# Optimization experiments

Hardware: AMD Instinct MI355X
Metric: run time of the kernel (lower is better)

The kernel has to match this reference:

```python
import jax, jax.numpy as jnp
import numpy as np

N_NODES = 50000
N_EDGES = 800000
IN_CH = 64
HID = 64
N_LAYERS = 4


def setup_inputs() -> dict:
    key = jax.random.key(0)
    ks = jax.random.split(key, 10)
    x = jax.random.normal(ks[0], (N_NODES, IN_CH), dtype=jnp.float32)
    edge_index = jax.random.randint(ks[1], (2, N_EDGES), 0, N_NODES, dtype=jnp.int32)
    # SAGEConv params per layer: lin_l (applied to aggregated neighbors, with bias)
    # and lin_r (applied to root node). All layers are 64->64 so stack to [L, in, out].
    s = 1.0 / np.sqrt(IN_CH)
    Wl = jax.random.uniform(ks[2], (N_LAYERS, IN_CH, HID), jnp.float32, -s, s)
    Wr = jax.random.uniform(ks[3], (N_LAYERS, IN_CH, HID), jnp.float32, -s, s)
    b = jax.random.uniform(ks[4], (N_LAYERS, HID), jnp.float32, -s, s)
    alpha = jnp.full((N_LAYERS, HID), 0.25, dtype=jnp.float32)  # PReLU init
    return {"x": x, "edge_index": edge_index, "Wl": Wl, "Wr": Wr, "b": b, "alpha": alpha}


def _sage_layer(x, src, dst, deg_inv, Wl, Wr, b):
    # mean aggregation of source-node features at destination nodes
    agg = jax.ops.segment_sum(x[src], dst, num_segments=N_NODES)  # [N, d]
    agg = agg * deg_inv[:, None]
    return agg @ Wl + x @ Wr + b


def _prelu(x, a):
    return jnp.where(x >= 0, x, a * x)


def reference(x, edge_index, Wl, Wr, b, alpha):
    src, dst = edge_index[0], edge_index[1]
    deg = jax.ops.segment_sum(jnp.ones((N_EDGES,), jnp.float32), dst, num_segments=N_NODES)
    deg_inv = 1.0 / jnp.maximum(deg, 1.0)
    for i in range(N_LAYERS):
        x = _sage_layer(x, src, dst, deg_inv, Wl[i], Wr[i], b[i])
        x = _prelu(x, alpha[i])
    return x
```

## Files before the change

### kernel.cpp

```cpp
#include <hip/hip_runtime.h>

#define NN 50000
#define NE 800000
#define C 64
#define NL 4
#define SCAN_NB 196
#define NBK 196
#define HBLK 782

typedef __attribute__((ext_vector_type(8))) short bf16x8;
typedef __attribute__((ext_vector_type(4))) float f32x4;

__device__ __forceinline__ unsigned short f2bf(float f) {
    unsigned u = __float_as_uint(f);
    u += 0x7fffu + ((u >> 16) & 1u);
    return (unsigned short)(u >> 16);
}
__device__ __forceinline__ float4 bf4_to_f4(uint2 p) {
    float4 r;
    r.x = __uint_as_float(p.x << 16);
    r.y = __uint_as_float(p.x & 0xffff0000u);
    r.z = __uint_as_float(p.y << 16);
    r.w = __uint_as_float(p.y & 0xffff0000u);
    return r;
}

__global__ __launch_bounds__(1024) void bucket_hist_kernel(const int* __restrict__ dst,
                                                           int* __restrict__ blk_cnt,
                                                           int* __restrict__ lrank) {
    __shared__ int cnt[NBK];
    int tid = threadIdx.x;
    int blk = blockIdx.x;
    if (tid < NBK) cnt[tid] = 0;
    __syncthreads();
    int e = blk * 1024 + tid;
    if (e < NE) lrank[e] = atomicAdd(&cnt[dst[e] >> 8], 1);
    __syncthreads();
    if (tid < NBK) blk_cnt[tid * HBLK + blk] = cnt[tid];
}

__global__ __launch_bounds__(1024) void scanblk_kernel(int* __restrict__ blk_cnt,
                                                       int* __restrict__ bucket_tot) {
    __shared__ int sdata[1024];
    int b = blockIdx.x;
    int tid = threadIdx.x;
    int v = (tid < HBLK) ? blk_cnt[b * HBLK + tid] : 0;
    sdata[tid] = v;
    __syncthreads();
    for (int off = 1; off < 1024; off <<= 1) {
        int t = (tid >= off) ? sdata[tid - off] : 0;
        __syncthreads();
        sdata[tid] += t;
        __syncthreads();
    }
    if (tid < HBLK) blk_cnt[b * HBLK + tid] = sdata[tid] - v;
    if (tid == HBLK - 1) bucket_tot[b] = sdata[tid];
}

__global__ __launch_bounds__(256) void scanbucket_kernel(const int* __restrict__ bucket_tot,
                                                         int* __restrict__ bucket_start) {
    __shared__ int sdata[256];
    int tid = threadIdx.x;
    int v = (tid < NBK) ? bucket_tot[tid] : 0;
    sdata[tid] = v;
    __syncthreads();
    for (int off = 1; off < 256; off <<= 1) {
        int t = (tid >= off) ? sdata[tid - off] : 0;
        __syncthreads();
        sdata[tid] += t;
        __syncthreads();
    }
    if (tid < NBK) bucket_start[tid] = sdata[tid] - v;
    if (tid == NBK - 1) bucket_start[NBK] = sdata[tid];
}

__global__ __launch_bounds__(1024) void bucket_scatter_kernel(
    const int* __restrict__ src, const int* __restrict__ dst,
    const int* __restrict__ lrank, const int* __restrict__ base2,
    const int* __restrict__ bucket_start, int2* __restrict__ sorted) {
    int blk = blockIdx.x;
    int e = blk * 1024 + threadIdx.x;
    if (e < NE) {
        int d = dst[e];
        int b = d >> 8;
        int pos = bucket_start[b] + base2[b * HBLK + blk] + lrank[e];
        sorted[pos] = make_int2(src[e], d);
    }
}

__global__ __launch_bounds__(512) void bucket_deg_kernel(const int2* __restrict__ sorted,
                                                         const int* __restrict__ bucket_start,
                                                         int* __restrict__ deg) {
    __shared__ int ldeg[256];
    int b = blockIdx.x;
    int tid = threadIdx.x;
    if (tid < 256) ldeg[tid] = 0;
    __syncthreads();
    int lo = bucket_start[b], hi = bucket_start[b + 1];
    for (int i = lo + tid; i < hi; i += 512)
        atomicAdd(&ldeg[sorted[i].y & 255], 1);
    __syncthreads();
    if (tid < 256) deg[b * 256 + tid] = ldeg[tid];
}

__global__ __launch_bounds__(256) void scan1_kernel(const int* __restrict__ deg,
                                                    int* __restrict__ row_start,
                                                    int* __restrict__ bsums) {
    __shared__ int sdata[256];
    int tid = threadIdx.x;
    int i = blockIdx.x * 256 + tid;
    int v = (i < NN) ? deg[i] : 0;
    sdata[tid] = v;
    __syncthreads();
    for (int off = 1; off < 256; off <<= 1) {
        int t = (tid >= off) ? sdata[tid - off] : 0;
        __syncthreads();
        sdata[tid] += t;
        __syncthreads();
    }
    int incl = sdata[tid];
    if (i < NN) row_start[i] = incl - v;
    if (tid == 255) bsums[blockIdx.x] = incl;
}

__global__ __launch_bounds__(256) void scan23_kernel(int* __restrict__ row_start,
                                                     const int* __restrict__ bsums,
                                                     const int* __restrict__ deg,
                                                     float* __restrict__ deg_inv) {
    __shared__ int sdata[256];
    int tid = threadIdx.x;
    int v = (tid < SCAN_NB) ? bsums[tid] : 0;
    sdata[tid] = v;
    __syncthreads();
    for (int off = 1; off < 256; off <<= 1) {
        int t = (tid >= off) ? sdata[tid - off] : 0;
        __syncthreads();
        sdata[tid] += t;
        __syncthreads();
    }
    int b = blockIdx.x;
    int offset = (b == 0) ? 0 : sdata[b - 1];
    int i = b * 256 + tid;
    if (i < NN) {
        row_start[i] += offset;
        deg_inv[i] = 1.0f / fmaxf((float)deg[i], 1.0f);
    }
}

__global__ __launch_bounds__(512) void bucket_fill_kernel(const int2* __restrict__ sorted,
                                                          const int* __restrict__ bucket_start,
                                                          const int* __restrict__ row_start,
                                                          int* __restrict__ csr_src) {
    __shared__ int rs[256];
    __shared__ int lcnt[256];
    int b = blockIdx.x;
    int tid = threadIdx.x;
    if (tid < 256) {
        int n = b * 256 + tid;
        rs[tid] = (n < NN) ? row_start[n] : 0;
        lcnt[tid] = 0;
    }
    __syncthreads();
    int lo = bucket_start[b], hi = bucket_start[b + 1];
    for (int i = lo + tid; i < hi; i += 512) {
        int2 p = sorted[i];
        int r = atomicAdd(&lcnt[p.y & 255], 1);
        csr_src[rs[p.y & 255] + r] = p.x;
    }
}

__global__ __launch_bounds__(512) void transform_mfma_kernel(
    const float* __restrict__ xin,
    const float* __restrict__ Wl, const float* __restrict__ Wr,
    const float* __restrict__ bias,
    unsigned short* __restrict__ y, float* __restrict__ z)
{
    __shared__ unsigned short xs[64][72];
    __shared__ unsigned short wlT[64][72];
    __shared__ unsigned short wrT[64][72];
    __shared__ unsigned short ys[64][64];
    __shared__ float zs[64][64];
    __shared__ float bs[C];

    int tid = threadIdx.x;
    int node0 = blockIdx.x * 64;

    for (int i = tid; i < C * C; i += 512) {
        int k = i >> 6, c = i & 63;
        wlT[c][k] = f2bf(Wl[i]);
        wrT[c][k] = f2bf(Wr[i]);
    }
    if (tid < C) bs[tid] = bias[tid];
    for (int i = tid; i < 64 * 16; i += 512) {
        int nl = i >> 4, c4 = i & 15;
        int n = node0 + nl;
        int nc = n < NN ? n : NN - 1;
        float4 v = ((const float4*)xin)[(size_t)nc * 16 + c4];
        xs[nl][c4 * 4 + 0] = f2bf(v.x);
        xs[nl][c4 * 4 + 1] = f2bf(v.y);
        xs[nl][c4 * 4 + 2] = f2bf(v.z);
        xs[nl][c4 * 4 + 3] = f2bf(v.w);
    }
    __syncthreads();

    int w = tid >> 6;
    int l = tid & 63;
    int mt = w >> 1;
    int half = w & 1;
    int r16 = l & 15;
    int kg = l >> 4;

    bf16x8 a0 = *(const bf16x8*)&xs[mt * 16 + r16][kg * 8];
    bf16x8 a1 = *(const bf16x8*)&xs[mt * 16 + r16][32 + kg * 8];

    f32x4 acc[4];
    #pragma unroll
    for (int nt = 0; nt < 4; nt++) {
        float bv = half ? bs[nt * 16 + r16] : 0.f;
        acc[nt] = (f32x4){bv, bv, bv, bv};
    }
    #pragma unroll
    for (int nt = 0; nt < 4; nt++) {
        const unsigned short* col = half ? &wrT[nt * 16 + r16][0] : &wlT[nt * 16 + r16][0];
        bf16x8 b0 = *(const bf16x8*)&col[kg * 8];
        bf16x8 b1 = *(const bf16x8*)&col[32 + kg * 8];
        acc[nt] = __builtin_amdgcn_mfma_f32_16x16x32_bf16(a0, b0, acc[nt], 0, 0, 0);
        acc[nt] = __builtin_amdgcn_mfma_f32_16x16x32_bf16(a1, b1, acc[nt], 0, 0, 0);
    }
    #pragma unroll
    for (int nt = 0; nt < 4; nt++) {
        #pragma unroll
        for (int j = 0; j < 4; j++) {
            int r = mt * 16 + kg * 4 + j;
            int c = nt * 16 + r16;
            if (half) zs[r][c] = acc[nt][j];
            else      ys[r][c] = f2bf(acc[nt][j]);
        }
    }
    __syncthreads();

    for (int i = tid; i < 64 * 16; i += 512) {
        int r = i >> 4, g = i & 15;
        int n = node0 + r;
        if (n < NN) {
            ((ushort4*)&y[(size_t)n * C])[g] = ((const ushort4*)&ys[r][0])[g];
            ((float4*)&z[(size_t)n * C])[g] = ((const float4*)&zs[r][0])[g];
        }
    }
}

__device__ __forceinline__ float4 gather_row(const uint2* __restrict__ yb,
                                             const int* __restrict__ cp, int d, int ql) {
    float4 acc = make_float4(0.f, 0.f, 0.f, 0.f);
    for (int t = 0; t < d; t += 8) {
        int lim = d - 1 - t;
        int j1 = min(1, lim), j2 = min(2, lim), j3 = min(3, lim);
        int j4 = min(4, lim), j5 = min(5, lim), j6 = min(6, lim), j7 = min(7, lim);
        float m1 = lim >= 1 ? 1.f : 0.f, m2 = lim >= 2 ? 1.f : 0.f;
        float m3 = lim >= 3 ? 1.f : 0.f, m4 = lim >= 4 ? 1.f : 0.f;
        float m5 = lim >= 5 ? 1.f : 0.f, m6 = lim >= 6 ? 1.f : 0.f;
        float m7 = lim >= 7 ? 1.f : 0.f;
        int s0 = cp[t];
        int s1 = cp[t + j1];
        int s2 = cp[t + j2];
        int s3 = cp[t + j3];
        int s4 = cp[t + j4];
        int s5 = cp[t + j5];
        int s6 = cp[t + j6];
        int s7 = cp[t + j7];
        uint2 p0 = yb[(size_t)s0 * 16 + ql];
        uint2 p1 = yb[(size_t)s1 * 16 + ql];
        uint2 p2 = yb[(size_t)s2 * 16 + ql];
        uint2 p3 = yb[(size_t)s3 * 16 + ql];
        uint2 p4 = yb[(size_t)s4 * 16 + ql];
        uint2 p5 = yb[(size_t)s5 * 16 + ql];
        uint2 p6 = yb[(size_t)s6 * 16 + ql];
        uint2 p7 = yb[(size_t)s7 * 16 + ql];
        float4 v0 = bf4_to_f4(p0);
        float4 v1 = bf4_to_f4(p1);
        float4 v2 = bf4_to_f4(p2);
        float4 v3 = bf4_to_f4(p3);
        float4 v4 = bf4_to_f4(p4);
        float4 v5 = bf4_to_f4(p5);
        float4 v6 = bf4_to_f4(p6);
        float4 v7 = bf4_to_f4(p7);
        acc.x += v0.x;      acc.y += v0.y;      acc.z += v0.z;      acc.w += v0.w;
        acc.x += v1.x * m1; acc.y += v1.y * m1; acc.z += v1.z * m1; acc.w += v1.w * m1;
        acc.x += v2.x * m2; acc.y += v2.y * m2; acc.z += v2.z * m2; acc.w += v2.w * m2;
        acc.x += v3.x * m3; acc.y += v3.y * m3; acc.z += v3.z * m3; acc.w += v3.w * m3;
        acc.x += v4.x * m4; acc.y += v4.y * m4; acc.z += v4.z * m4; acc.w += v4.w * m4;
        acc.x += v5.x * m5; acc.y += v5.y * m5; acc.z += v5.z * m5; acc.w += v5.w * m5;
        acc.x += v6.x * m6; acc.y += v6.y * m6; acc.z += v6.z * m6; acc.w += v6.w * m6;
        acc.x += v7.x * m7; acc.y += v7.y * m7; acc.z += v7.z * m7; acc.w += v7.w * m7;
    }
    return acc;
}

__global__ __launch_bounds__(512) void fused_gt_kernel(
    const uint2* __restrict__ yb, const float4* __restrict__ z4,
    const int* __restrict__ row_start, const int* __restrict__ deg,
    const float* __restrict__ deg_inv, const float* __restrict__ alpha,
    const int* __restrict__ csr_src,
    const float* __restrict__ Wl2, const float* __restrict__ Wr2,
    const float* __restrict__ bias2,
    unsigned short* __restrict__ yout, float* __restrict__ zout)
{
    __shared__ unsigned short wlT[64][72];
    __shared__ unsigned short wrT[64][72];
    __shared__ unsigned short xsb[32][72];
    __shared__ unsigned short ys[32][64];
    __shared__ float zs[32][64];
    __shared__ float bs2[C];

    int tid = threadIdx.x;
    for (int i = tid; i < C * C; i += 512) {
        int k = i >> 6, c = i & 63;
        wlT[c][k] = f2bf(Wl2[i]);
        wrT[c][k] = f2bf(Wr2[i]);
    }
    if (tid < C) bs2[tid] = bias2[tid];

    int nl = tid >> 4;
    int ql = tid & 15;
    int n = blockIdx.x * 32 + nl;

    float4 o = make_float4(0.f, 0.f, 0.f, 0.f);
    if (n < NN) {
        int rs = row_start[n];
        int d = deg[n];
        float4 acc = gather_row(yb, csr_src + rs, d, ql);
        float di = deg_inv[n];
        float4 zz = z4[(size_t)n * 16 + ql];
        float4 a4 = ((const float4*)alpha)[ql];
        o.x = di * acc.x + zz.x;
        o.y = di * acc.y + zz.y;
        o.z = di * acc.z + zz.z;
        o.w = di * acc.w + zz.w;
        o.x = o.x >= 0.f ? o.x : a4.x * o.x;
        o.y = o.y >= 0.f ? o.y : a4.y * o.y;
        o.z = o.z >= 0.f ? o.z : a4.z * o.z;
        o.w = o.w >= 0.f ? o.w : a4.w * o.w;
    }
    {
        ushort4 p = make_ushort4(f2bf(o.x), f2bf(o.y), f2bf(o.z), f2bf(o.w));
        *(ushort4*)&xsb[nl][ql * 4] = p;
    }
    __syncthreads();

    int w = tid >> 6;
    int l = tid & 63;
    int mt = w & 1;
    int half = (w >> 1) & 1;
    int ntg = w >> 2;
    int r16 = l & 15;
    int kg = l >> 4;

    bf16x8 a0 = *(const bf16x8*)&xsb[mt * 16 + r16][kg * 8];
    bf16x8 a1 = *(const bf16x8*)&xsb[mt * 16 + r16][32 + kg * 8];

    #pragma unroll
    for (int q = 0; q < 2; q++) {
        int nt = ntg * 2 + q;
        const unsigned short* col = half ? &wrT[nt * 16 + r16][0] : &wlT[nt * 16 + r16][0];
        bf16x8 b0 = *(const bf16x8*)&col[kg * 8];
        bf16x8 b1 = *(const bf16x8*)&col[32 + kg * 8];
        float bv = half ? bs2[nt * 16 + r16] : 0.f;
        f32x4 acc = (f32x4){bv, bv, bv, bv};
        acc = __builtin_amdgcn_mfma_f32_16x16x32_bf16(a0, b0, acc, 0, 0, 0);
        acc = __builtin_amdgcn_mfma_f32_16x16x32_bf16(a1, b1, acc, 0, 0, 0);
        #pragma unroll
        for (int j = 0; j < 4; j++) {
            int r = mt * 16 + kg * 4 + j;
            int c = nt * 16 + r16;
            if (half) zs[r][c] = acc[j];
            else      ys[r][c] = f2bf(acc[j]);
        }
    }
    __syncthreads();

    {
        int r = tid >> 4, g = tid & 15;
        int n2 = blockIdx.x * 32 + r;
        if (n2 < NN) {
            ((ushort4*)&yout[(size_t)n2 * C])[g] = ((const ushort4*)&ys[r][0])[g];
            ((float4*)&zout[(size_t)n2 * C])[g] = ((const float4*)&zs[r][0])[g];
        }
    }
}

__global__ __launch_bounds__(256) void gather_kernel(
    const uint2* __restrict__ yb, const float4* __restrict__ z4,
    const int* __restrict__ row_start, const int* __restrict__ deg,
    const float* __restrict__ deg_inv, const float* __restrict__ alpha,
    const int* __restrict__ csr_src,
    float4* __restrict__ out4)
{
    int tid = threadIdx.x;
    int n = blockIdx.x * 16 + (tid >> 4);
    int ql = tid & 15;

    int rs = row_start[n];
    int d = deg[n];
    float4 acc = gather_row(yb, csr_src + rs, d, ql);

    float di = deg_inv[n];
    float4 zz = z4[(size_t)n * 16 + ql];
    float4 a4 = ((const float4*)alpha)[ql];
    float4 o;
    o.x = di * acc.x + zz.x;
    o.y = di * acc.y + zz.y;
    o.z = di * acc.z + zz.z;
    o.w = di * acc.w + zz.w;
    o.x = o.x >= 0.f ? o.x : a4.x * o.x;
    o.y = o.y >= 0.f ? o.y : a4.y * o.y;
    o.z = o.z >= 0.f ? o.z : a4.z * o.z;
    o.w = o.w >= 0.f ? o.w : a4.w * o.w;
    out4[(size_t)n * 16 + ql] = o;
}

extern "C" void kernel_launch(void* const* d_in, const int* in_sizes, int n_in,
                              void* d_out, int out_size, void* d_ws, size_t ws_size,
                              hipStream_t stream) {
    const float* x     = (const float*)d_in[0];
    const int*   ei    = (const int*)d_in[1];
    const float* Wl    = (const float*)d_in[2];
    const float* Wr    = (const float*)d_in[3];
    const float* b     = (const float*)d_in[4];
    const float* alpha = (const float*)d_in[5];
    float* out = (float*)d_out;

    const int* src = ei;
    const int* dst = ei + NE;

    char* wsp = (char*)d_ws;
    int*  lrank        = (int*)wsp;                 wsp += (size_t)NE * 4;
    int*  blk_cnt      = (int*)wsp;                 wsp += (size_t)NBK * HBLK * 4 + 256;
    int*  bucket_tot   = (int*)wsp;                 wsp += 1024;
    int*  bucket_start = (int*)wsp;                 wsp += 1024;
    int2* sorted       = (int2*)wsp;                wsp += (size_t)NE * 8;
    int*  deg          = (int*)wsp;                 wsp += (size_t)(NBK * 256) * 4;
    float* deg_inv     = (float*)wsp;               wsp += (size_t)NN * 4;
    int*  row_start    = (int*)wsp;                 wsp += (size_t)NN * 4;
    int*  bsums        = (int*)wsp;                 wsp += 1024;
    unsigned short* y0buf = (unsigned short*)wsp;   wsp += (size_t)NN * C * 2;
    unsigned short* y1buf = (unsigned short*)wsp;   wsp += (size_t)NN * C * 2;
    float* z0buf       = (float*)wsp;               wsp += (size_t)NN * C * 4;
    float* z1buf       = (float*)wsp;
    int*  csr_src      = lrank;

    bucket_hist_kernel<<<HBLK, 1024, 0, stream>>>(dst, blk_cnt, lrank);
    scanblk_kernel<<<NBK, 1024, 0, stream>>>(blk_cnt, bucket_tot);
    scanbucket_kernel<<<1, 256, 0, stream>>>(bucket_tot, bucket_start);
    bucket_scatter_kernel<<<HBLK, 1024, 0, stream>>>(src, dst, lrank, blk_cnt,
                                                     bucket_start, sorted);
    bucket_deg_kernel<<<NBK, 512, 0, stream>>>(sorted, bucket_start, deg);
    scan1_kernel<<<SCAN_NB, 256, 0, stream>>>(deg, row_start, bsums);
    scan23_kernel<<<SCAN_NB, 256, 0, stream>>>(row_start, bsums, deg, deg_inv);
    bucket_fill_kernel<<<NBK, 512, 0, stream>>>(sorted, bucket_start, row_start, csr_src);

    transform_mfma_kernel<<<(NN + 63) / 64, 512, 0, stream>>>(x, Wl, Wr, b, y0buf, z0buf);

    const int fblocks = (NN + 31) / 32;
    unsigned short* ycur = y0buf; float* zcur = z0buf;
    unsigned short* ynxt = y1buf; float* znxt = z1buf;
    for (int l = 0; l < NL - 1; l++) {
        fused_gt_kernel<<<fblocks, 512, 0, stream>>>(
            (const uint2*)ycur, (const float4*)zcur,
            row_start, deg, deg_inv, alpha + (size_t)l * C, csr_src,
            Wl + (size_t)(l + 1) * C * C, Wr + (size_t)(l + 1) * C * C,
            b + (size_t)(l + 1) * C,
            ynxt, znxt);
        unsigned short* ty = ycur; float* tz = zcur;
        ycur = ynxt; zcur = znxt;
        ynxt = ty;   znxt = tz;
    }

    gather_kernel<<<NN / 16, 256, 0, stream>>>(
        (const uint2*)ycur, (const float4*)zcur, row_start, deg,
        deg_inv, alpha + (size_t)(NL - 1) * C, csr_src, (float4*)out);
}
```

Baseline: 163.9 us.

## Fuse CSR-build scan and bucket kernels into scatter and one finalize kernel

Removes the standalone bucket-scan, degree, two global scan and fill kernels. Each scatter and finalize block redundantly scans the 196 bucket totals in shared memory, and the finalize kernel computes per-node degrees, local prefix offsets, row_start, deg_inv and the CSR fill in one pass. This cuts five kernel launches and their global round trips. The cost is a redundant 256-wide scan repeated in every block.

```diff
diff --git a/kernel.cpp b/kernel.cpp
--- a/kernel.cpp
+++ b/kernel.cpp
@@ -4,7 +4,6 @@
 #define NE 800000
 #define C 64
 #define NL 4
-#define SCAN_NB 196
 #define NBK 196
 #define HBLK 782
 
@@ -57,115 +56,100 @@
     if (tid == HBLK - 1) bucket_tot[b] = sdata[tid];
 }
 
-__global__ __launch_bounds__(256) void scanbucket_kernel(const int* __restrict__ bucket_tot,
-                                                         int* __restrict__ bucket_start) {
-    __shared__ int sdata[256];
-    int tid = threadIdx.x;
-    int v = (tid < NBK) ? bucket_tot[tid] : 0;
-    sdata[tid] = v;
-    __syncthreads();
-    for (int off = 1; off < 256; off <<= 1) {
-        int t = (tid >= off) ? sdata[tid - off] : 0;
-        __syncthreads();
-        sdata[tid] += t;
-        __syncthreads();
-    }
-    if (tid < NBK) bucket_start[tid] = sdata[tid] - v;
-    if (tid == NBK - 1) bucket_start[NBK] = sdata[tid];
-}
-
 __global__ __launch_bounds__(1024) void bucket_scatter_kernel(
     const int* __restrict__ src, const int* __restrict__ dst,
     const int* __restrict__ lrank, const int* __restrict__ base2,
-    const int* __restrict__ bucket_start, int2* __restrict__ sorted) {
+    const int* __restrict__ bucket_tot, int2* __restrict__ sorted) {
+    __shared__ int sscan[256];
+    __shared__ int sex[256];
+    int tid = threadIdx.x;
     int blk = blockIdx.x;
-    int e = blk * 1024 + threadIdx.x;
+    int v0 = 0;
+    if (tid < 256) {
+        v0 = (tid < NBK) ? bucket_tot[tid] : 0;
+        sscan[tid] = v0;
+    }
+    __syncthreads();
+    for (int off = 1; off < 256; off <<= 1) {
+        int t = (tid < 256 && tid >= off) ? sscan[tid - off] : 0;
+        __syncthreads();
+        if (tid < 256) sscan[tid] += t;
+        __syncthreads();
+    }
+    if (tid < 256) sex[tid] = sscan[tid] - v0;
+    __syncthreads();
+
+    int e = blk * 1024 + tid;
     if (e < NE) {
         int d = dst[e];
         int b = d >> 8;
-        int pos = bucket_start[b] + base2[b * HBLK + blk] + lrank[e];
+        int pos = sex[b] + base2[b * HBLK + blk] + lrank[e];
         sorted[pos] = make_int2(src[e], d);
     }
 }
 
-__global__ __launch_bounds__(512) void bucket_deg_kernel(const int2* __restrict__ sorted,
-                                                         const int* __restrict__ bucket_start,
-                                                         int* __restrict__ deg) {
+__global__ __launch_bounds__(512) void bucket_finalize_kernel(
+    const int2* __restrict__ sorted, const int* __restrict__ bucket_tot,
+    int* __restrict__ row_start, int* __restrict__ deg, float* __restrict__ deg_inv,
+    int* __restrict__ csr_src) {
+    __shared__ int sscan[256];
     __shared__ int ldeg[256];
+    __shared__ int lpre[256];
+    __shared__ int lcnt[256];
+
     int b = blockIdx.x;
     int tid = threadIdx.x;
-    if (tid < 256) ldeg[tid] = 0;
-    __syncthreads();
-    int lo = bucket_start[b], hi = bucket_start[b + 1];
+    int v0 = 0;
+    if (tid < 256) {
+        v0 = (tid < NBK) ? bucket_tot[tid] : 0;
+        sscan[tid] = v0;
+        ldeg[tid] = 0;
+        lcnt[tid] = 0;
+    }
+    __syncthreads();
+    for (int off = 1; off < 256; off <<= 1) {
+        int t = (tid < 256 && tid >= off) ? sscan[tid - off] : 0;
+        __syncthreads();
+        if (tid < 256) sscan[tid] += t;
+        __syncthreads();
+    }
+    int lo = (b == 0) ? 0 : sscan[b - 1];
+    int hi = sscan[b];
+    __syncthreads();
+
     for (int i = lo + tid; i < hi; i += 512)
         atomicAdd(&ldeg[sorted[i].y & 255], 1);
     __syncthreads();
-    if (tid < 256) deg[b * 256 + tid] = ldeg[tid];
-}
-
-__global__ __launch_bounds__(256) void scan1_kernel(const int* __restrict__ deg,
-                                                    int* __restrict__ row_start,
-                                                    int* __restrict__ bsums) {
-    __shared__ int sdata[256];
-    int tid = threadIdx.x;
-    int i = blockIdx.x * 256 + tid;
-    int v = (i < NN) ? deg[i] : 0;
-    sdata[tid] = v;
+
+    int dv = 0;
+    if (tid < 256) {
+        dv = ldeg[tid];
+        lpre[tid] = dv;
+    }
     __syncthreads();
     for (int off = 1; off < 256; off <<= 1) {
-        int t = (tid >= off) ? sdata[tid - off] : 0;
-        __syncthreads();
-        sdata[tid] += t;
-        __syncthreads();
-    }
-    int incl = sdata[tid];
-    if (i < NN) row_start[i] = incl - v;
-    if (tid == 255) bsums[blockIdx.x] = incl;
-}
-
-__global__ __launch_bounds__(256) void scan23_kernel(int* __restrict__ row_start,
-                                                     const int* __restrict__ bsums,
-                                                     const int* __restrict__ deg,
-                                                     float* __restrict__ deg_inv) {
-    __shared__ int sdata[256];
-    int tid = threadIdx.x;
-    int v = (tid < SCAN_NB) ? bsums[tid] : 0;
-    sdata[tid] = v;
-    __syncthreads();
-    for (int off = 1; off < 256; off <<= 1) {
-        int t = (tid >= off) ? sdata[tid - off] : 0;
-        __syncthreads();
-        sdata[tid] += t;
-        __syncthreads();
-    }
-    int b = blockIdx.x;
-    int offset = (b == 0) ? 0 : sdata[b - 1];
-    int i = b * 256 + tid;
-    if (i < NN) {
-        row_start[i] += offset;
-        deg_inv[i] = 1.0f / fmaxf((float)deg[i], 1.0f);
-    }
-}
-
-__global__ __launch_bounds__(512) void bucket_fill_kernel(const int2* __restrict__ sorted,
-                                                          const int* __restrict__ bucket_start,
-                                                          const int* __restrict__ row_start,
-                                                          int* __restrict__ csr_src) {
-    __shared__ int rs[256];
-    __shared__ int lcnt[256];
-    int b = blockIdx.x;
-    int tid = threadIdx.x;
+        int t = (tid < 256 && tid >= off) ? lpre[tid - off] : 0;
+        __syncthreads();
+        if (tid < 256) lpre[tid] += t;
+        __syncthreads();
+    }
     if (tid < 256) {
+        int p = lpre[tid] - dv;
+        lpre[tid] = p;
         int n = b * 256 + tid;
-        rs[tid] = (n < NN) ? row_start[n] : 0;
-        lcnt[tid] = 0;
-    }
-    __syncthreads();
-    int lo = bucket_start[b], hi = bucket_start[b + 1];
+        if (n < NN) {
+            row_start[n] = lo + p;
+            deg[n] = dv;
+            deg_inv[n] = 1.0f / fmaxf((float)dv, 1.0f);
+        }
+    }
+    __syncthreads();
+
     for (int i = lo + tid; i < hi; i += 512) {
         int2 p = sorted[i];
-        int r = atomicAdd(&lcnt[p.y & 255], 1);
-        csr_src[rs[p.y & 255] + r] = p.x;
+        int loc = p.y & 255;
+        int r = atomicAdd(&lcnt[loc], 1);
+        csr_src[lo + lpre[loc] + r] = p.x;
     }
 }
 
@@ -436,12 +420,10 @@
     int*  lrank        = (int*)wsp;                 wsp += (size_t)NE * 4;
     int*  blk_cnt      = (int*)wsp;                 wsp += (size_t)NBK * HBLK * 4 + 256;
     int*  bucket_tot   = (int*)wsp;                 wsp += 1024;
-    int*  bucket_start = (int*)wsp;                 wsp += 1024;
     int2* sorted       = (int2*)wsp;                wsp += (size_t)NE * 8;
     int*  deg          = (int*)wsp;                 wsp += (size_t)(NBK * 256) * 4;
     float* deg_inv     = (float*)wsp;               wsp += (size_t)NN * 4;
     int*  row_start    = (int*)wsp;                 wsp += (size_t)NN * 4;
-    int*  bsums        = (int*)wsp;                 wsp += 1024;
     unsigned short* y0buf = (unsigned short*)wsp;   wsp += (size_t)NN * C * 2;
     unsigned short* y1buf = (unsigned short*)wsp;   wsp += (size_t)NN * C * 2;
     float* z0buf       = (float*)wsp;               wsp += (size_t)NN * C * 4;
@@ -450,13 +432,10 @@
 
     bucket_hist_kernel<<<HBLK, 1024, 0, stream>>>(dst, blk_cnt, lrank);
     scanblk_kernel<<<NBK, 1024, 0, stream>>>(blk_cnt, bucket_tot);
-    scanbucket_kernel<<<1, 256, 0, stream>>>(bucket_tot, bucket_start);
     bucket_scatter_kernel<<<HBLK, 1024, 0, stream>>>(src, dst, lrank, blk_cnt,
-                                                     bucket_start, sorted);
-    bucket_deg_kernel<<<NBK, 512, 0, stream>>>(sorted, bucket_start, deg);
-    scan1_kernel<<<SCAN_NB, 256, 0, stream>>>(deg, row_start, bsums);
-    scan23_kernel<<<SCAN_NB, 256, 0, stream>>>(row_start, bsums, deg, deg_inv);
-    bucket_fill_kernel<<<NBK, 512, 0, stream>>>(sorted, bucket_start, row_start, csr_src);
+                                                     bucket_tot, sorted);
+    bucket_finalize_kernel<<<NBK, 512, 0, stream>>>(sorted, bucket_tot,
+                                                    row_start, deg, deg_inv, csr_src);
 
     transform_mfma_kernel<<<(NN + 63) / 64, 512, 0, stream>>>(x, Wl, Wr, b, y0buf, z0buf);
 
```

After: 158.3 us. -3.4%, faster.
